# Performance work log

Hardware: AMD Instinct MI355X
Metric: run time of the kernel (lower is better)

## Reference

```python
import jax, jax.numpy as jnp
import numpy as np

B = 8192
D = 1024
NUM_CLASSES = 100


def setup_inputs() -> dict:
    key = jax.random.key(0)
    kx, ky = jax.random.split(key)
    x = jax.random.normal(kx, (B, D), dtype=jnp.float32)
    y = jax.random.randint(ky, (B,), 0, NUM_CLASSES, dtype=jnp.int64)
    return {"x": x, "y": y, "T": 1}


def reference(x, y, T):
    b = x.shape[0]
    # Pairwise Euclidean distances via Gram matrix (same math as
    # torch.norm(x[:,None]-x, dim=2) without the b*b*d intermediate).
    xn = jnp.sum(x * x, axis=1)                      # [b]
    d2 = xn[None, :] + xn[:, None] - 2.0 * (x @ x.T)  # [b, b]
    d2 = jnp.maximum(d2, 0.0)
    eye = jnp.eye(b, dtype=bool)
    # Diagonal is masked to -inf below; plug 1.0 to keep sqrt well-defined.
    dist = jnp.sqrt(jnp.where(eye, 1.0, d2))
    e_dist = -dist * T
    neg_inf = jnp.float32(-jnp.inf)
    # Denominator: all pairs except self.
    den_dist = jnp.where(eye, neg_inf, e_dist)
    # Numerator: same-label pairs except self.
    same = (y[None, :] == y[:, None]) & ~eye
    num_dist = jnp.where(same, e_dist, neg_inf)
    num = jax.nn.logsumexp(num_dist, axis=1)         # [b]
    den = jax.nn.logsumexp(den_dist, axis=1)         # [b]
    # Original fixup: anchors with no positives (num == -inf) contribute 0 to num;
    # den is re-indexed by isinf(num) AFTER num was zeroed, so den is unchanged.
    num = jnp.where(jnp.isinf(num), 0.0, num)
    return -jnp.mean(num - den)
```

## Files before the change

### kernel.cpp

```cpp
#include <hip/hip_runtime.h>
#include <hip/hip_bf16.h>
#include <stdint.h>

#define BN 8192
#define DK 1024
#define NT 16
#define NTILES 2080

typedef __attribute__((ext_vector_type(4))) float f32x4;
typedef __attribute__((ext_vector_type(2))) long long2v;

#define BAR() do { asm volatile("" ::: "memory"); __builtin_amdgcn_s_barrier(); asm volatile("" ::: "memory"); } while (0)

__device__ __forceinline__ unsigned int f2e4m3(float f) {
  const unsigned int u = __float_as_uint(f);
  const unsigned int sign = (u >> 24) & 0x80u;
  float a = fabsf(f);
  if (a >= 448.f) return sign | 0x7Eu;
  if (a < 0.015625f) {
    int m = (int)rintf(a * 512.f);
    return sign | (unsigned int)m;
  }
  unsigned int x = __float_as_uint(a);
  x += 0x7FFFFu + ((x >> 20) & 1u);
  const unsigned int e = (x >> 23) - 127u + 7u;
  const unsigned int m = (x >> 20) & 7u;
  return sign | (e << 4) | m;
}

__global__ __launch_bounds__(256) void snn_prep(const float* __restrict__ x,
                                                unsigned char* __restrict__ xb,
                                                float* __restrict__ xn,
                                                float* __restrict__ den,
                                                float* __restrict__ num,
                                                float* __restrict__ out) {
  const int row = blockIdx.x * 4 + (threadIdx.x >> 6);
  const int lane = threadIdx.x & 63;
  const float4* src = (const float4*)(x + (size_t)row * DK) + lane * 4;
  float s = 0.f;
  unsigned int pk[4];
#pragma unroll
  for (int i = 0; i < 4; ++i) {
    float4 v = src[i];
    s = fmaf(v.x, v.x, s); s = fmaf(v.y, v.y, s);
    s = fmaf(v.z, v.z, s); s = fmaf(v.w, v.w, s);
    pk[i] = f2e4m3(v.x) | (f2e4m3(v.y) << 8) | (f2e4m3(v.z) << 16) |
            (f2e4m3(v.w) << 24);
  }
  const int g = lane >> 2;
  const int c = lane & 3;
  uint4 o; o.x = pk[0]; o.y = pk[1]; o.z = pk[2]; o.w = pk[3];
  *(uint4*)(xb + (size_t)row * DK + g * 64 + ((c ^ ((row >> 1) & 3)) << 4)) = o;
#pragma unroll
  for (int m = 32; m >= 1; m >>= 1) s += __shfl_xor(s, m);
  if (lane == 0) {
    xn[row] = s;
    den[row] = 0.f;
    num[row] = 0.f;
    if (row == 0) out[0] = 0.f;
  }
}

__global__ __launch_bounds__(256, 3) void snn_main(
    const unsigned char* __restrict__ xb, const float* __restrict__ xn,
    const int* __restrict__ y, const unsigned int* __restrict__ Tp,
    float* __restrict__ den, float* __restrict__ num) {
  __shared__ __align__(16) unsigned char As[3][128 * 64];
  __shared__ __align__(16) unsigned char Bs[3][128 * 64];
  __shared__ float xnA[128], xnB[128];
  __shared__ int yA[128], yB[128];

  const int t = threadIdx.x;
  const int lane = t & 63;
  const int w = t >> 6;
  const int wr = w >> 1, wc = w & 1;
  const int l15 = lane & 15;
  const int lg = lane >> 4;

  const int bid = blockIdx.x;
  const int ts = (bid & 7) * (NTILES / 8) + (bid >> 3);
  int I = (int)(64.5f - sqrtf(64.5f * 64.5f - 2.0f * (float)ts));
  while (I > 0 && (64 * I - (I * (I - 1)) / 2) > ts) --I;
  while ((64 * (I + 1) - ((I + 1) * I) / 2) <= ts) ++I;
  const int J = I + (ts - (64 * I - (I * (I - 1)) / 2));
  const int r0 = I * 128, c0 = J * 128;
  const bool diag = (I == J);

  const unsigned int tu = *Tp;
  const float tf = (tu & 0x7f800000u) ? __uint_as_float(tu) : (float)(int)tu;

  if (t < 128) {
    xnA[t] = xn[r0 + t]; yA[t] = y[r0 + t];
    xnB[t] = xn[c0 + t]; yB[t] = y[c0 + t];
  }

  auto ISSUE = [&](int buf, int kt) {
#pragma unroll
    for (int i = 0; i < 2; ++i) {
      const int linear = i * 256 + t;
      const int row = linear >> 2;
      const int cg = linear & 3;
      const unsigned char* sa = xb + (size_t)(r0 + row) * DK + kt + cg * 16;
      const unsigned char* sb = xb + (size_t)(c0 + row) * DK + kt + cg * 16;
      __builtin_amdgcn_global_load_lds(
          (const __attribute__((address_space(1))) void*)sa,
          (__attribute__((address_space(3))) void*)(As[buf] + linear * 16), 16, 0, 0);
      __builtin_amdgcn_global_load_lds(
          (const __attribute__((address_space(1))) void*)sb,
          (__attribute__((address_space(3))) void*)(Bs[buf] + linear * 16), 16, 0, 0);
    }
  };

  f32x4 acc[4][4];
#pragma unroll
  for (int mi = 0; mi < 4; ++mi)
#pragma unroll
    for (int ni = 0; ni < 4; ++ni) acc[mi][ni] = (f32x4){0.f, 0.f, 0.f, 0.f};

  const int fro = (lg ^ ((l15 >> 1) & 3)) << 4;
  const int rowA[4] = {(wr * 64 + 0 * 16 + l15) * 64, (wr * 64 + 1 * 16 + l15) * 64,
                       (wr * 64 + 2 * 16 + l15) * 64, (wr * 64 + 3 * 16 + l15) * 64};
  const int rowB[4] = {(wc * 64 + 0 * 16 + l15) * 64, (wc * 64 + 1 * 16 + l15) * 64,
                       (wc * 64 + 2 * 16 + l15) * 64, (wc * 64 + 3 * 16 + l15) * 64};

  long2v aF[2][4], bF[2][4];

  ISSUE(0, 0);
  ISSUE(1, 64);
  asm volatile("s_waitcnt vmcnt(4)" ::: "memory");
  BAR();
#pragma unroll
  for (int mi = 0; mi < 4; ++mi) aF[0][mi] = *(const long2v*)(As[0] + rowA[mi] + fro);
#pragma unroll
  for (int ni = 0; ni < 4; ++ni) bF[0][ni] = *(const long2v*)(Bs[0] + rowB[ni] + fro);

#pragma unroll
  for (int T = 0; T < NT; ++T) {
    const int cb = T & 1;
    if (T + 2 < NT) {
      ISSUE((T + 2) % 3, (T + 2) * 64);
      asm volatile("s_waitcnt vmcnt(4)" ::: "memory");
    } else if (T + 1 < NT) {
      asm volatile("s_waitcnt vmcnt(0)" ::: "memory");
    }
    if (T + 1 < NT) {
      const int nrd = (T + 1) % 3;
      const int nb = (T + 1) & 1;
#pragma unroll
      for (int mi = 0; mi < 4; ++mi)
        aF[nb][mi] = *(const long2v*)(As[nrd] + rowA[mi] + fro);
#pragma unroll
      for (int ni = 0; ni < 4; ++ni)
        bF[nb][ni] = *(const long2v*)(Bs[nrd] + rowB[ni] + fro);
    }
    __builtin_amdgcn_s_setprio(1);
#pragma unroll
    for (int kk = 0; kk < 2; ++kk)
#pragma unroll
      for (int mi = 0; mi < 4; ++mi)
#pragma unroll
        for (int ni = 0; ni < 4; ++ni)
          acc[mi][ni] = __builtin_amdgcn_mfma_f32_16x16x32_fp8_fp8(
              aF[cb][mi][kk], bF[cb][ni][kk], acc[mi][ni], 0, 0, 0);
    __builtin_amdgcn_s_setprio(0);
    if (T + 1 < NT) BAR();
  }

  float cxn[4]; int cy[4];
#pragma unroll
  for (int ni = 0; ni < 4; ++ni) {
    const int c_l = wc * 64 + ni * 16 + l15;
    cxn[ni] = xnB[c_l]; cy[ni] = yB[c_l];
  }
#pragma unroll
  for (int mi = 0; mi < 4; ++mi) {
#pragma unroll
    for (int rg = 0; rg < 4; ++rg) {
      const int row_l = wr * 64 + mi * 16 + lg * 4 + rg;
      const int rG = r0 + row_l;
      const float rxn = xnA[row_l];
      const int ry = yA[row_l];
      float u = 0.f, av = 0.f;
#pragma unroll
      for (int ni = 0; ni < 4; ++ni) {
        const int cG = c0 + wc * 64 + ni * 16 + l15;
        const float a = acc[mi][ni][rg];
        const float d2 = fmaxf(rxn + cxn[ni] - 2.0f * a, 0.f);
        const float p = (rG == cG) ? 0.f : __expf(-sqrtf(d2) * tf);
        const float v = (ry == cy[ni]) ? -p : p;
        acc[mi][ni][rg] = v;
        u += v; av += fabsf(v);
      }
#pragma unroll
      for (int mm = 8; mm >= 1; mm >>= 1) {
        u += __shfl_xor(u, mm); av += __shfl_xor(av, mm);
      }
      if (l15 == 0) {
        atomicAdd(&den[rG], av);
        atomicAdd(&num[rG], 0.5f * (av - u));
      }
    }
  }
  if (!diag) {
#pragma unroll
    for (int ni = 0; ni < 4; ++ni) {
      float u = 0.f, av = 0.f;
#pragma unroll
      for (int mi = 0; mi < 4; ++mi)
#pragma unroll
        for (int rg = 0; rg < 4; ++rg) {
          const float v = acc[mi][ni][rg];
          u += v; av += fabsf(v);
        }
      u += __shfl_xor(u, 16); av += __shfl_xor(av, 16);
      u += __shfl_xor(u, 32); av += __shfl_xor(av, 32);
      if (lg == 0) {
        const int cG = c0 + wc * 64 + ni * 16 + l15;
        atomicAdd(&den[cG], av);
        atomicAdd(&num[cG], 0.5f * (av - u));
      }
    }
  }
}

__global__ __launch_bounds__(256) void snn_final(const float* __restrict__ den,
                                                 const float* __restrict__ num,
                                                 float* __restrict__ out) {
  __shared__ float red[256];
  const int t = threadIdx.x;
  const int r = blockIdx.x * 256 + t;
  const float sd = den[r], sn = num[r];
  const float d = logf(sd);
  const float n = (sn > 0.f) ? logf(sn) : 0.f;
  red[t] = d - n;
  __syncthreads();
  for (int s = 128; s >= 1; s >>= 1) {
    if (t < s) red[t] += red[t + s];
    __syncthreads();
  }
  if (t == 0) atomicAdd(out, red[0] * (1.0f / (float)BN));
}

extern "C" void kernel_launch(void* const* d_in, const int* in_sizes, int n_in,
                              void* d_out, int out_size, void* d_ws, size_t ws_size,
                              hipStream_t stream) {
  const float* x = (const float*)d_in[0];
  const int* y = (const int*)d_in[1];
  const unsigned int* Tp = (const unsigned int*)d_in[2];
  float* out = (float*)d_out;

  char* ws = (char*)d_ws;
  unsigned char* xb = (unsigned char*)ws;
  float* xn = (float*)(ws + (size_t)BN * DK);
  float* den = xn + BN;
  float* num = den + BN;

  snn_prep<<<dim3(BN / 4), dim3(256), 0, stream>>>(x, xb, xn, den, num, out);
  snn_main<<<dim3(NTILES), dim3(256), 0, stream>>>(xb, xn, y, Tp, den, num);
  snn_final<<<dim3(32), dim3(256), 0, stream>>>(den, num, out);
}
```

Before: 105.0 us.

## Software-pipeline LDS fragment reads with inline asm ds_read overlapping prior-tile MFMAs

Restructures the K loop so each iteration issues ds_read_b128 loads for the current tile through inline assembly, then runs the MFMAs for the previous tile's fragments while those reads are in flight. An explicit lgkmcnt wait and a sched_barrier control ordering, and a final MFMA block drains the last tile after the loop. The goal is to hide LDS read latency behind matrix instructions, at the cost of manual waitcnt correctness risk and fixed buffer-offset arithmetic.

```diff
diff --git a/kernel.cpp b/kernel.cpp
--- a/kernel.cpp
+++ b/kernel.cpp
@@ -11,6 +11,12 @@
 typedef __attribute__((ext_vector_type(2))) long long2v;
 
 #define BAR() do { asm volatile("" ::: "memory"); __builtin_amdgcn_s_barrier(); asm volatile("" ::: "memory"); } while (0)
+
+__device__ __forceinline__ long2v dsr128(unsigned addr) {
+  long2v r;
+  asm volatile("ds_read_b128 %0, %1" : "=v"(r) : "v"(addr));
+  return r;
+}
 
 __device__ __forceinline__ unsigned int f2e4m3(float f) {
   const unsigned int u = __float_as_uint(f);
@@ -118,53 +124,65 @@
     for (int ni = 0; ni < 4; ++ni) acc[mi][ni] = (f32x4){0.f, 0.f, 0.f, 0.f};
 
   const int fro = (lg ^ ((l15 >> 1) & 3)) << 4;
-  const int rowA[4] = {(wr * 64 + 0 * 16 + l15) * 64, (wr * 64 + 1 * 16 + l15) * 64,
-                       (wr * 64 + 2 * 16 + l15) * 64, (wr * 64 + 3 * 16 + l15) * 64};
-  const int rowB[4] = {(wc * 64 + 0 * 16 + l15) * 64, (wc * 64 + 1 * 16 + l15) * 64,
-                       (wc * 64 + 2 * 16 + l15) * 64, (wc * 64 + 3 * 16 + l15) * 64};
+  const unsigned asB = (unsigned)(size_t)(__attribute__((address_space(3))) unsigned char*)&As[0][0];
+  const unsigned bsB = (unsigned)(size_t)(__attribute__((address_space(3))) unsigned char*)&Bs[0][0];
+  unsigned aOff[4], bOff[4];
+#pragma unroll
+  for (int mi = 0; mi < 4; ++mi) aOff[mi] = (unsigned)((wr * 64 + mi * 16 + l15) * 64 + fro);
+#pragma unroll
+  for (int ni = 0; ni < 4; ++ni) bOff[ni] = (unsigned)((wc * 64 + ni * 16 + l15) * 64 + fro);
 
   long2v aF[2][4], bF[2][4];
 
   ISSUE(0, 0);
   ISSUE(1, 64);
   asm volatile("s_waitcnt vmcnt(4)" ::: "memory");
+  asm volatile("s_waitcnt lgkmcnt(0)" ::: "memory");
   BAR();
-#pragma unroll
-  for (int mi = 0; mi < 4; ++mi) aF[0][mi] = *(const long2v*)(As[0] + rowA[mi] + fro);
-#pragma unroll
-  for (int ni = 0; ni < 4; ++ni) bF[0][ni] = *(const long2v*)(Bs[0] + rowB[ni] + fro);
 
 #pragma unroll
   for (int T = 0; T < NT; ++T) {
-    const int cb = T & 1;
+    const int cb = T & 1, pb = cb ^ 1;
+    const unsigned aBuf = asB + (unsigned)((T % 3) * 8192);
+    const unsigned bBuf = bsB + (unsigned)((T % 3) * 8192);
+#pragma unroll
+    for (int mi = 0; mi < 4; ++mi) aF[cb][mi] = dsr128(aBuf + aOff[mi]);
+#pragma unroll
+    for (int ni = 0; ni < 4; ++ni) bF[cb][ni] = dsr128(bBuf + bOff[ni]);
     if (T + 2 < NT) {
       ISSUE((T + 2) % 3, (T + 2) * 64);
       asm volatile("s_waitcnt vmcnt(4)" ::: "memory");
-    } else if (T + 1 < NT) {
+    } else if (T == NT - 2) {
       asm volatile("s_waitcnt vmcnt(0)" ::: "memory");
     }
-    if (T + 1 < NT) {
-      const int nrd = (T + 1) % 3;
-      const int nb = (T + 1) & 1;
-#pragma unroll
-      for (int mi = 0; mi < 4; ++mi)
-        aF[nb][mi] = *(const long2v*)(As[nrd] + rowA[mi] + fro);
+    if (T > 0) {
+      asm volatile("s_waitcnt lgkmcnt(8)" ::: "memory");
+      __builtin_amdgcn_sched_barrier(0);
+      __builtin_amdgcn_s_setprio(1);
+#pragma unroll
+      for (int kk = 0; kk < 2; ++kk)
+#pragma unroll
+        for (int mi = 0; mi < 4; ++mi)
+#pragma unroll
+          for (int ni = 0; ni < 4; ++ni)
+            acc[mi][ni] = __builtin_amdgcn_mfma_f32_16x16x32_fp8_fp8(
+                aF[pb][mi][kk], bF[pb][ni][kk], acc[mi][ni], 0, 0, 0);
+      __builtin_amdgcn_s_setprio(0);
+    }
+    if (T < NT - 1) BAR();
+  }
+  asm volatile("s_waitcnt lgkmcnt(0)" ::: "memory");
+  __builtin_amdgcn_sched_barrier(0);
+  __builtin_amdgcn_s_setprio(1);
+#pragma unroll
+  for (int kk = 0; kk < 2; ++kk)
+#pragma unroll
+    for (int mi = 0; mi < 4; ++mi)
 #pragma unroll
       for (int ni = 0; ni < 4; ++ni)
-        bF[nb][ni] = *(const long2v*)(Bs[nrd] + rowB[ni] + fro);
-    }
-    __builtin_amdgcn_s_setprio(1);
-#pragma unroll
-    for (int kk = 0; kk < 2; ++kk)
-#pragma unroll
-      for (int mi = 0; mi < 4; ++mi)
-#pragma unroll
-        for (int ni = 0; ni < 4; ++ni)
-          acc[mi][ni] = __builtin_amdgcn_mfma_f32_16x16x32_fp8_fp8(
-              aF[cb][mi][kk], bF[cb][ni][kk], acc[mi][ni], 0, 0, 0);
-    __builtin_amdgcn_s_setprio(0);
-    if (T + 1 < NT) BAR();
-  }
+        acc[mi][ni] = __builtin_amdgcn_mfma_f32_16x16x32_fp8_fp8(
+            aF[1][mi][kk], bF[1][ni][kk], acc[mi][ni], 0, 0, 0);
+  __builtin_amdgcn_s_setprio(0);
 
   float cxn[4]; int cy[4];
 #pragma unroll
```

Measured after the change: 110.1 us. 1.05x slower.
